# Performance work log

Measured on AMD Instinct MI355X. Metric: run time of the kernel, lower is better.

The kernel has to match this reference:

```python
import jax, jax.numpy as jnp
import numpy as np

L = 19          # kernel size (hardcoded 19x19 views in the original)
HH = WW = 256   # hardcoded fold output_size=(256,256)


def _patches(x, l):
    # x: (Hp, Wp) -> (H, W, l, l) sliding windows (stride 1, valid)
    h = x.shape[0] - l + 1
    w = x.shape[1] - l + 1
    r = jnp.arange(h)[:, None] + jnp.arange(l)[None, :]   # (h, l)
    c = jnp.arange(w)[:, None] + jnp.arange(l)[None, :]   # (w, l)
    return x[r[:, None, :, None], c[None, :, None, :]]    # (h, w, l, l)


def setup_inputs() -> dict:
    key = jax.random.key(0)
    k1, k2 = jax.random.split(key)
    inp = jax.random.normal(k1, (1, 3, HH, WW), dtype=jnp.float32)
    ker = jax.random.uniform(k2, (L, L, HH, WW), dtype=jnp.float32)
    return {"input": inp, "kernel": ker}


def _forward(inp, ker):
    l = L
    B, C, h, w = inp.shape  # B must be 1 (original reshapes assume it)
    p2 = l // 2
    pad = jnp.pad(inp, ((0, 0), (0, 0), (p2, p2), (p2, p2)), mode="reflect")
    k = ker
    out_unf = None
    for i in range(3):  # replicates the original channel loop (only last kept)
        p = _patches(pad[0, i], l)                        # (h, w, l, l)
        # torch F.unfold layout: (l*l kernel-pos row-major, h*w spatial row-major)
        unf = p.transpose(2, 3, 0, 1).reshape(l * l, h * w)
        # torch: (1, l*l, h*w) -> reshape(1, h*w, 1, l, l); row-major reflatten
        dg = unf.reshape(h * w, l, l)
        # kernel: permute(2,3,0,1) + contiguous().view(-1,1,l,l), reassigned
        # each iteration exactly as in the original module
        k = jnp.transpose(k, (2, 3, 0, 1)).reshape(-1, 1, l, l)
        k = k / jnp.sum(k, axis=(1, 2, 3), keepdims=True)
        # grouped conv with one group per pixel on (l,l) patch == per-pixel dot
        out = jnp.einsum("pab,pab->p", dg, k[:, 0])       # (h*w,)
        out_unf = out.reshape(1, 1, h, w)                 # fold with k=1
    return out_unf


def reference(input, kernel):
    return _forward(input, kernel)
```

## Files before the change

kernel.cpp:

```cpp
#include <hip/hip_runtime.h>

#define NPIX 65536
#define KK   361
#define LSZ  19
#define HWD  256
#define QB   16
#define CT   4
#define CHUNK 64
#define GPART (NPIX / CHUNK)
#define NTHR 512
#define NSLOT 8
#define NS2  16
#define SPS2 23
#define DTC  82

__device__ __forceinline__ int refl(int v) {
    v -= 9;
    v = v < 0 ? -v : v;
    v = v > 255 ? 510 - v : v;
    return v;
}

__global__ __launch_bounds__(256) void k_s1a(const float4* __restrict__ ker4,
                                             float4* __restrict__ part4) {
    const int p4 = blockIdx.x * 256 + threadIdx.x;
    const int strip = blockIdx.y;
    const int s0 = strip * SPS2;
    const int n = (strip == NS2 - 1) ? (KK - s0) : SPS2;
    const float4* kp = ker4 + (size_t)s0 * (NPIX / 4) + p4;
    float4 acc = {0.f, 0.f, 0.f, 0.f};
#pragma unroll 8
    for (int s = 0; s < n; ++s) {
        float4 v = kp[(size_t)s * (NPIX / 4)];
        acc.x += v.x; acc.y += v.y; acc.z += v.z; acc.w += v.w;
    }
    part4[(size_t)strip * (NPIX / 4) + p4] = acc;
}

__global__ __launch_bounds__(256) void k_s1b(const float4* __restrict__ part4,
                                             float4* __restrict__ rcp4) {
    const int i = blockIdx.x * 256 + threadIdx.x;
    float4 a = {0.f, 0.f, 0.f, 0.f};
#pragma unroll
    for (int s = 0; s < NS2; ++s) {
        float4 v = part4[(size_t)s * (NPIX / 4) + i];
        a.x += v.x; a.y += v.y; a.z += v.z; a.w += v.w;
    }
    rcp4[i] = float4{1.0f / a.x, 1.0f / a.y, 1.0f / a.z, 1.0f / a.w};
}

__global__ __launch_bounds__(NTHR) void k_part(const float* __restrict__ ker,
                                               const float* __restrict__ rcpS1,
                                               const float* __restrict__ in2,
                                               float2* __restrict__ partial) {
    switch (blockIdx.x >> 8) {
        case 1: __builtin_amdgcn_s_sleep(10); break;
        case 2: __builtin_amdgcn_s_sleep(20); break;
        case 3: __builtin_amdgcn_s_sleep(30); break;
        default: break;
    }

    __shared__ float tile[QB * KK];
    __shared__ float dt[LSZ * DTC];
    __shared__ float rcpS2s[QB];
    const int tid = threadIdx.x;
    const int lb  = ((blockIdx.x & 7) << 7) | (blockIdx.x >> 3);
    const int q0  = lb * CHUNK;

    {
        const int y0 = q0 >> 8, x0 = q0 & 255;
        for (int i = tid; i < LSZ * DTC; i += NTHR) {
            int ai = i / DTC, ci = i - ai * DTC;
            dt[i] = in2[refl(y0 + ai) * HWD + refl(x0 + ci)];
        }
    }

    const int t  = tid;
    const int j0 = t * NPIX + q0;
    const int r0 = j0 / KK;
    const int jm = j0 - r0 * KK;
    const int d0 = (jm == 0) ? CHUNK : (KK - jm);
    const int split = d0 < CHUNK ? d0 : CHUNK;
    const int la = t / LSZ, lb2 = t - LSZ * la;
    const int dbase = la * DTC + lb2;
    float ad = 0.f, as = 0.f, sd = 0.f, ss = 0.f;
    const int wave = tid >> 6, lane = tid & 63;
    const int half = lane >> 5, l32 = lane & 31;

    for (int k = 0; k < CT; ++k) {
        __syncthreads();
        const int basek = (q0 + k * QB) * KK;
        const float4* k4 = (const float4*)(ker + basek);
        for (int i = tid; i < (QB * KK) / 4; i += NTHR) {
            float4 v = k4[i];
            int m = basek + i * 4;
            const float4 s = *(const float4*)(rcpS1 + (m & (NPIX - 1)));
            v.x *= s.x; v.y *= s.y; v.z *= s.z; v.w *= s.w;
            *(float4*)(tile + i * 4) = v;
        }
        __syncthreads();
        {
            const int row = 2 * wave + half;
            float acc = 0.f;
            for (int e = l32; e < KK; e += 32) acc += tile[row * KK + e];
            acc += __shfl_xor(acc, 1);
            acc += __shfl_xor(acc, 2);
            acc += __shfl_xor(acc, 4);
            acc += __shfl_xor(acc, 8);
            acc += __shfl_xor(acc, 16);
            if (l32 == 0) rcpS2s[row] = 1.0f / acc;
        }
        __syncthreads();
        if (t < KK) {
#pragma unroll
            for (int o = 0; o < QB; ++o) {
                const int off = k * QB + o;
                if (off == split) { sd = ad; ss = as; }
                float v = tile[o * KK + t] * rcpS2s[o];
                float d = dt[dbase + off];
                ad += d * v;
                as += v;
            }
        }
    }

    if (t < KK) {
        const int slot = lb & (NSLOT - 1);
        if (split == CHUNK) {
            partial[(size_t)r0 * NSLOT + slot] = float2{ad, as};
        } else {
            partial[(size_t)r0 * NSLOT + slot] = float2{sd, ss};
            partial[(size_t)(r0 + 1) * NSLOT + slot] = float2{ad - sd, as - ss};
        }
    }
}

__global__ __launch_bounds__(256) void k_out2(const float2* __restrict__ partial,
                                              float* __restrict__ out) {
    const int r = blockIdx.x * 256 + threadIdx.x;
    const int j0 = r * KK;
    const int qs = j0 & (NPIX - 1);
    const int ql = (j0 + KK - 1) & (NPIX - 1);
    const int first = qs >> 6;
    const int last  = ql >> 6;
    const int cnt = ((last - first) & (GPART - 1)) + 1;
    const float2* p = partial + (size_t)r * NSLOT;
    float dot = 0.f, sum = 0.f;
    for (int i = 0; i < cnt; ++i) {
        float2 v = p[(first + i) & (NSLOT - 1)];
        dot += v.x; sum += v.y;
    }
    out[r] = dot / sum;
}

__global__ __launch_bounds__(256) void k_s1(const float* __restrict__ ker,
                                            float* __restrict__ rcpS1) {
    int p = blockIdx.x * blockDim.x + threadIdx.x;
    const float* kp = ker + p;
    float a = 0.f;
    for (int s = 0; s < KK; ++s) a += kp[(size_t)s * NPIX];
    rcpS1[p] = 1.0f / a;
}

__global__ __launch_bounds__(256) void k_s2_fallback(const float* __restrict__ ker,
                                                     const float* __restrict__ rcpS1,
                                                     float* __restrict__ rcpS2) {
    int lane = threadIdx.x & 63;
    int q = blockIdx.x * 4 + (threadIdx.x >> 6);
    int base = q * KK;
    float acc = 0.f;
    for (int t = lane; t < KK; t += 64)
        acc += ker[base + t] * rcpS1[(base + t) & (NPIX - 1)];
    for (int m = 1; m < 64; m <<= 1) acc += __shfl_xor(acc, m);
    if (lane == 0) rcpS2[q] = 1.0f / acc;
}

__global__ __launch_bounds__(256) void k_out_fallback(const float* __restrict__ ker,
                                                      const float* __restrict__ rcpS1,
                                                      const float* __restrict__ rcpS2,
                                                      const float* __restrict__ in2,
                                                      float* __restrict__ out) {
    int lane = threadIdx.x & 63;
    int r = blockIdx.x * 4 + (threadIdx.x >> 6);
    float vsum = 0.f, vdot = 0.f;
    for (int u = lane; u < KK; u += 64) {
        int jj = r * KK + u;
        int t  = jj >> 16;
        int q  = jj & (NPIX - 1);
        int m  = q * KK + t;
        float v = ker[m] * rcpS1[m & (NPIX - 1)] * rcpS2[q];
        int y = q >> 8, x = q & 255;
        int a = t / LSZ, b = t - a * LSZ;
        float d = in2[refl(y + a) * HWD + refl(x + b)];
        vsum += v;
        vdot += d * v;
    }
    for (int mm = 1; mm < 64; mm <<= 1) {
        vsum += __shfl_xor(vsum, mm);
        vdot += __shfl_xor(vdot, mm);
    }
    if (lane == 0) out[r] = vdot / vsum;
}

extern "C" void kernel_launch(void* const* d_in, const int* in_sizes, int n_in,
                              void* d_out, int out_size, void* d_ws, size_t ws_size,
                              hipStream_t stream) {
    const float* inp = (const float*)d_in[0];
    const float* ker = (const float*)d_in[1];
    float* out = (float*)d_out;
    const float* in2 = inp + 2 * NPIX;

    float*  rcpS1   = (float*)d_ws;
    float*  s1part  = rcpS1 + NPIX;
    float2* partial = (float2*)(s1part + (size_t)NS2 * NPIX);

    const size_t needed = ((size_t)NPIX * (1 + NS2) +
                           (size_t)NPIX * NSLOT * 2) * sizeof(float);

    if (ws_size >= needed) {
        dim3 g1(NPIX / 4 / 256, NS2);
        k_s1a<<<g1, 256, 0, stream>>>((const float4*)ker, (float4*)s1part);
        k_s1b<<<NPIX / 4 / 256, 256, 0, stream>>>((const float4*)s1part, (float4*)rcpS1);
        k_part<<<GPART, NTHR, 0, stream>>>(ker, rcpS1, in2, partial);
        k_out2<<<NPIX / 256, 256, 0, stream>>>(partial, out);
    } else {
        float* rcpS2 = rcpS1 + NPIX;
        k_s1<<<NPIX / 256, 256, 0, stream>>>(ker, rcpS1);
        k_s2_fallback<<<NPIX / 4, 256, 0, stream>>>(ker, rcpS1, rcpS2);
        k_out_fallback<<<NPIX / 4, 256, 0, stream>>>(ker, rcpS1, rcpS2, in2, out);
    }
}
```

Before: 45.49 us.

## Double-buffer kernel tiles in k_part with register prefetch of next chunk

The k_part loop now keeps two shared-memory tile buffers. It issues the global loads (kernel plus reciprocal row sums) for the next 16-pixel chunk into registers before computing on the current chunk, then scales and stores them into the other buffer afterwards. The first tile and its normalisation are hoisted before the loop, which cuts one barrier per iteration and hides global load latency behind the dot-product work. It also adds an occupancy hint to launch_bounds. In exchange it doubles the tile's shared memory and raises register pressure, which may reduce how many blocks fit on each CU.

```diff
diff --git a/kernel.cpp b/kernel.cpp
--- a/kernel.cpp
+++ b/kernel.cpp
@@ -9,6 +9,7 @@
 #define CHUNK 64
 #define GPART (NPIX / CHUNK)
 #define NTHR 512
+#define NG4  ((QB * KK) / 4)
 #define NSLOT 8
 #define NS2  16
 #define SPS2 23
@@ -49,10 +50,10 @@
     rcp4[i] = float4{1.0f / a.x, 1.0f / a.y, 1.0f / a.z, 1.0f / a.w};
 }
 
-__global__ __launch_bounds__(NTHR) void k_part(const float* __restrict__ ker,
-                                               const float* __restrict__ rcpS1,
-                                               const float* __restrict__ in2,
-                                               float2* __restrict__ partial) {
+__global__ __launch_bounds__(NTHR, 6) void k_part(const float* __restrict__ ker,
+                                                  const float* __restrict__ rcpS1,
+                                                  const float* __restrict__ in2,
+                                                  float2* __restrict__ partial) {
     switch (blockIdx.x >> 8) {
         case 1: __builtin_amdgcn_s_sleep(10); break;
         case 2: __builtin_amdgcn_s_sleep(20); break;
@@ -60,12 +61,15 @@
         default: break;
     }
 
-    __shared__ float tile[QB * KK];
+    __shared__ float tile[2][QB * KK];
     __shared__ float dt[LSZ * DTC];
     __shared__ float rcpS2s[QB];
     const int tid = threadIdx.x;
     const int lb  = ((blockIdx.x & 7) << 7) | (blockIdx.x >> 3);
     const int q0  = lb * CHUNK;
+    const int wave = tid >> 6, lane = tid & 63;
+    const int half = lane >> 5, l32 = lane & 31;
+    const float4* rcp4 = (const float4*)rcpS1;
 
     {
         const int y0 = q0 >> 8, x0 = q0 & 255;
@@ -74,6 +78,31 @@
             dt[i] = in2[refl(y0 + ai) * HWD + refl(x0 + ci)];
         }
     }
+    {
+        const int base0 = q0 * KK;
+        const float4* k4 = (const float4*)(ker + base0);
+#pragma unroll
+        for (int j = 0; j < 3; ++j) {
+            const int i = tid + j * NTHR;
+            if (i < NG4) {
+                float4 v = k4[i];
+                const float4 s = rcp4[((base0 + i * 4) & (NPIX - 1)) >> 2];
+                v.x *= s.x; v.y *= s.y; v.z *= s.z; v.w *= s.w;
+                *(float4*)(&tile[0][i * 4]) = v;
+            }
+        }
+    }
+    __syncthreads();
+    {
+        const int row = 2 * wave + half;
+        float acc = 0.f;
+        for (int e = l32; e < KK; e += 32) acc += tile[0][row * KK + e];
+        acc += __shfl_xor(acc, 1);  acc += __shfl_xor(acc, 2);
+        acc += __shfl_xor(acc, 4);  acc += __shfl_xor(acc, 8);
+        acc += __shfl_xor(acc, 16);
+        if (l32 == 0) rcpS2s[row] = 1.0f / acc;
+    }
+    __syncthreads();
 
     const int t  = tid;
     const int j0 = t * NPIX + q0;
@@ -84,43 +113,53 @@
     const int la = t / LSZ, lb2 = t - LSZ * la;
     const int dbase = la * DTC + lb2;
     float ad = 0.f, as = 0.f, sd = 0.f, ss = 0.f;
-    const int wave = tid >> 6, lane = tid & 63;
-    const int half = lane >> 5, l32 = lane & 31;
-
+
+#pragma unroll
     for (int k = 0; k < CT; ++k) {
-        __syncthreads();
-        const int basek = (q0 + k * QB) * KK;
-        const float4* k4 = (const float4*)(ker + basek);
-        for (int i = tid; i < (QB * KK) / 4; i += NTHR) {
-            float4 v = k4[i];
-            int m = basek + i * 4;
-            const float4 s = *(const float4*)(rcpS1 + (m & (NPIX - 1)));
-            v.x *= s.x; v.y *= s.y; v.z *= s.z; v.w *= s.w;
-            *(float4*)(tile + i * 4) = v;
-        }
-        __syncthreads();
-        {
-            const int row = 2 * wave + half;
-            float acc = 0.f;
-            for (int e = l32; e < KK; e += 32) acc += tile[row * KK + e];
-            acc += __shfl_xor(acc, 1);
-            acc += __shfl_xor(acc, 2);
-            acc += __shfl_xor(acc, 4);
-            acc += __shfl_xor(acc, 8);
-            acc += __shfl_xor(acc, 16);
-            if (l32 == 0) rcpS2s[row] = 1.0f / acc;
-        }
-        __syncthreads();
+        float4 kv0, kv1, kv2, sv0, sv1, sv2;
+        int i0 = 0, i1 = 0, i2 = 0;
+        if (k < CT - 1) {
+            const int basek = (q0 + (k + 1) * QB) * KK;
+            const float4* k4 = (const float4*)(ker + basek);
+            i0 = tid;            i1 = tid + NTHR;       i2 = tid + 2 * NTHR;
+            kv0 = k4[i0];        sv0 = rcp4[((basek + i0 * 4) & (NPIX - 1)) >> 2];
+            kv1 = k4[i1];        sv1 = rcp4[((basek + i1 * 4) & (NPIX - 1)) >> 2];
+            if (i2 < NG4) {
+                kv2 = k4[i2];    sv2 = rcp4[((basek + i2 * 4) & (NPIX - 1)) >> 2];
+            }
+        }
         if (t < KK) {
+            const float* bc = tile[k & 1];
 #pragma unroll
             for (int o = 0; o < QB; ++o) {
                 const int off = k * QB + o;
                 if (off == split) { sd = ad; ss = as; }
-                float v = tile[o * KK + t] * rcpS2s[o];
+                float v = bc[o * KK + t] * rcpS2s[o];
                 float d = dt[dbase + off];
                 ad += d * v;
                 as += v;
             }
+        }
+        if (k < CT - 1) {
+            float* bn = tile[(k + 1) & 1];
+            kv0.x *= sv0.x; kv0.y *= sv0.y; kv0.z *= sv0.z; kv0.w *= sv0.w;
+            *(float4*)(&bn[i0 * 4]) = kv0;
+            kv1.x *= sv1.x; kv1.y *= sv1.y; kv1.z *= sv1.z; kv1.w *= sv1.w;
+            *(float4*)(&bn[i1 * 4]) = kv1;
+            if (i2 < NG4) {
+                kv2.x *= sv2.x; kv2.y *= sv2.y; kv2.z *= sv2.z; kv2.w *= sv2.w;
+                *(float4*)(&bn[i2 * 4]) = kv2;
+            }
+            __syncthreads();
+            const float* bn2 = tile[(k + 1) & 1];
+            const int row = 2 * wave + half;
+            float acc = 0.f;
+            for (int e = l32; e < KK; e += 32) acc += bn2[row * KK + e];
+            acc += __shfl_xor(acc, 1);  acc += __shfl_xor(acc, 2);
+            acc += __shfl_xor(acc, 4);  acc += __shfl_xor(acc, 8);
+            acc += __shfl_xor(acc, 16);
+            if (l32 == 0) rcpS2s[row] = 1.0f / acc;
+            __syncthreads();
         }
     }
 
```

Result: slower. 47.45 us, median of 2 (+4.3%).
